# Kernel tuning notes

Hardware: AMD Instinct MI355X
Metric: run time of the kernel (lower is better)

Reference implementation:

```python
import jax, jax.numpy as jnp
import numpy as np

DIM = 2048
HEADS = 16
HD = DIM // HEADS  # 128
EPS = 1e-5


def layernorm(t, w, b):
    # FloatLayerNorm: LayerNorm computed in float32 over last dim
    t32 = t.astype(jnp.float32)
    mu = jnp.mean(t32, axis=-1, keepdims=True)
    var = jnp.mean(jnp.square(t32 - mu), axis=-1, keepdims=True)
    y = (t32 - mu) * jax.lax.rsqrt(var + EPS)
    return (y * w + b).astype(t.dtype)


def rope(t, f_real, f_imag):
    # t: [b, s, h, hd]; frequencies in cis form, sliced to seq length
    b, s, h, hd = t.shape
    tr = t.astype(jnp.float32).reshape(b, s, h, hd // 2, 2)
    xr, xi = tr[..., 0], tr[..., 1]
    fr = f_real[:s][None, :, None, :]  # [1, s, 1, hd/2]
    fi = f_imag[:s][None, :, None, :]
    o_r = xr * fr - xi * fi
    o_i = xr * fi + xi * fr
    return jnp.stack([o_r, o_i], axis=-1).reshape(b, s, h, hd).astype(t.dtype)


def proj_norm_rope(t, Wq, Wk, Wv, qn_w, qn_b, kn_w, kn_b, f_real, f_imag):
    b, s, _ = t.shape
    q = layernorm(t @ Wq, qn_w, qn_b).reshape(b, s, HEADS, HD)
    k = layernorm(t @ Wk, kn_w, kn_b).reshape(b, s, HEADS, HD)
    v = (t @ Wv).reshape(b, s, HEADS, HD)
    q = rope(q, f_real, f_imag)
    k = rope(k, f_real, f_imag)
    return q, k, v


def sdpa(q, k, v, scale):
    # q,k,v: [b, s, h, hd] -> out [b, s, h, hd]
    scores = jnp.einsum('bqhd,bkhd->bhqk', q, k) * scale
    probs = jax.nn.softmax(scores, axis=-1)
    return jnp.einsum('bhqk,bkhd->bqhd', probs, v)


def setup_inputs() -> dict:
    key = jax.random.key(0)
    ks = jax.random.split(key, 14)
    d = {
        'c': jax.random.normal(ks[0], (2, 256, DIM), jnp.float32),
        'x': jax.random.normal(ks[1], (2, 1792, DIM), jnp.float32),
        'f_real': jax.random.normal(ks[2], (2048, HD // 2), jnp.float32),
        'f_imag': jax.random.normal(ks[3], (2048, HD // 2), jnp.float32),
    }
    sc = 1.0 / np.sqrt(DIM)
    for i, name in enumerate(['Wq', 'Wk', 'Wv', 'Wo', 'W2q', 'W2k', 'W2v', 'W2o']):
        d[name] = jax.random.normal(ks[4 + i], (DIM, DIM), jnp.float32) * sc
    for name in ['qn_w', 'kn_w', 'q2n_w', 'k2n_w']:
        d[name] = jnp.ones((DIM,), jnp.float32)
    for name in ['qn_b', 'kn_b', 'q2n_b', 'k2n_b']:
        d[name] = jnp.zeros((DIM,), jnp.float32)
    return d


def reference(c, x, f_real, f_imag, Wq, Wk, Wv, Wo, W2q, W2k, W2v, W2o,
              qn_w, qn_b, kn_w, kn_b, q2n_w, q2n_b, k2n_w, k2n_b):
    s1 = c.shape[1]
    c_q, c_k, c_v = proj_norm_rope(c, Wq, Wk, Wv, qn_w, qn_b, kn_w, kn_b, f_real, f_imag)
    x_q, x_k, x_v = proj_norm_rope(x, W2q, W2k, W2v, q2n_w, q2n_b, k2n_w, k2n_b, f_real, f_imag)
    q = jnp.concatenate([c_q, x_q], axis=1)
    k = jnp.concatenate([c_k, x_k], axis=1)
    v = jnp.concatenate([c_v, x_v], axis=1)
    out = sdpa(q, k, v, scale=1.0 / np.sqrt(HD))  # scale_by_num_heads=True
    b, s, _, _ = out.shape
    out = out.reshape(b, s, DIM)
    c_out = out[:, :s1] @ Wo
    x_out = out[:, s1:] @ W2o
    return c_out, x_out
```

## Files before the change

### kernel.cpp

```cpp
#include <hip/hip_runtime.h>

typedef __attribute__((ext_vector_type(8))) short short8;
typedef __attribute__((ext_vector_type(4))) float f32x4;
typedef __attribute__((ext_vector_type(16))) float f32x16;

#define DEV __device__ __forceinline__

DEV unsigned short f2bf(float f) {
  unsigned int u; __builtin_memcpy(&u, &f, 4);
  u = (u + 0x7FFFu + ((u >> 16) & 1u)) >> 16;
  return (unsigned short)u;
}
DEV float bf2f(unsigned short h) {
  unsigned int u = ((unsigned int)h) << 16;
  float f; __builtin_memcpy(&f, &u, 4);
  return f;
}
DEV unsigned int cvtpk(float lo, float hi_) {
  unsigned int r;
  asm("v_cvt_pk_bf16_f32 %0, %1, %2" : "=v"(r) : "v"(lo), "v"(hi_));
  return r;
}

DEV void gload_lds16(const void* g, void* l) {
  __builtin_amdgcn_global_load_lds(
      (const __attribute__((address_space(1))) void*)g,
      (__attribute__((address_space(3))) void*)l, 16, 0, 0);
}

DEV f32x16 mfma32(short8 a, short8 b, f32x16 c) {
  return __builtin_amdgcn_mfma_f32_32x32x16_bf16(a, b, c, 0, 0, 0);
}
DEV f32x4 mfma16(short8 a, short8 b, f32x4 c) {
  return __builtin_amdgcn_mfma_f32_16x16x32_bf16(a, b, c, 0, 0, 0);
}

__global__ __launch_bounds__(256) void conv_tb(const float* __restrict__ c,
                                               const float* __restrict__ x,
                                               unsigned short* __restrict__ tb) {
  int row = blockIdx.x;
  int b = row >> 11, s = row & 2047;
  const float* src = (s < 256) ? (c + (size_t)(b * 256 + s) * 2048)
                               : (x + (size_t)(b * 1792 + (s - 256)) * 2048);
  int t = threadIdx.x;
  float4 v0 = *(const float4*)&src[t * 8];
  float4 v1 = *(const float4*)&src[t * 8 + 4];
  union { unsigned short us[8]; uint4 u; } pk;
  pk.us[0] = f2bf(v0.x); pk.us[1] = f2bf(v0.y); pk.us[2] = f2bf(v0.z); pk.us[3] = f2bf(v0.w);
  pk.us[4] = f2bf(v1.x); pk.us[5] = f2bf(v1.y); pk.us[6] = f2bf(v1.z); pk.us[7] = f2bf(v1.w);
  *(uint4*)&tb[(size_t)row * 2048 + t * 8] = pk.u;
}

__global__ __launch_bounds__(256) void trans_w(
    const float* __restrict__ w0, const float* __restrict__ w1,
    const float* __restrict__ w2, const float* __restrict__ w3,
    const float* __restrict__ w4, const float* __restrict__ w5,
    const float* __restrict__ w6, const float* __restrict__ w7,
    unsigned short* __restrict__ dstbase) {
  const float* W;
  switch (blockIdx.z) {
    case 0: W = w0; break; case 1: W = w1; break; case 2: W = w2; break; case 3: W = w3; break;
    case 4: W = w4; break; case 5: W = w5; break; case 6: W = w6; break; default: W = w7; break;
  }
  unsigned short* Wt = dstbase + (size_t)blockIdx.z * 2048 * 2048;
  __shared__ float tile[64][65];
  int n0 = blockIdx.x * 64, k0 = blockIdx.y * 64;
  int j = threadIdx.x & 63, i0 = threadIdx.x >> 6;
#pragma unroll
  for (int p = 0; p < 16; ++p) {
    int i = i0 + p * 4;
    tile[i][j] = W[(size_t)(k0 + i) * 2048 + n0 + j];
  }
  __syncthreads();
#pragma unroll
  for (int p = 0; p < 16; ++p) {
    int i = i0 + p * 4;
    Wt[(size_t)(n0 + i) * 2048 + k0 + j] = f2bf(tile[j][i]);
  }
}

DEV void stage_A8(char* ldsAbase, const unsigned short* gtile, int mh, int wid, int lane) {
#pragma unroll
  for (int p = 0; p < 2; ++p) {
    int row0 = mh * 64 + p * 128 + wid * 8;
    int row = row0 + (lane >> 3);
    int u = (lane & 7) ^ (row & 7);
    gload_lds16(gtile + (size_t)row * 2048 + u * 8, ldsAbase + row0 * 128);
  }
}
DEV void stage_B8(char* ldsBbase, const unsigned short* gtile, int nh, int wid, int lane) {
#pragma unroll
  for (int p = 0; p < 2; ++p) {
    int idx = p * 8 + wid;
    int row0 = (idx >> 2) * 64 + nh * 32 + (idx & 3) * 8;
    int row = row0 + (lane >> 3);
    int u = (lane & 7) ^ (row & 7);
    gload_lds16(gtile + (size_t)row * 2048 + u * 8, ldsBbase + row0 * 128);
  }
}

__global__ __launch_bounds__(512, 2) void gemm_qkv3_8ph(
    const unsigned short* __restrict__ A,
    const unsigned short* __restrict__ Wt,
    unsigned short* __restrict__ out) {
  extern __shared__ __align__(16) char ldsc[];
  const size_t M2 = 2048ull * 2048ull;
  int bid = blockIdx.x;
  int sw = (bid & 7) * 48 + (bid >> 3);
  const int which = sw >> 7;
  const int rem = sw & 127;
  const int m0 = (rem >> 3) * 256, n0 = (rem & 7) * 256;
  const unsigned short* Bt = Wt + (size_t)(((m0 & 2047) < 256) ? which : which + 4) * M2;
  unsigned short* C = out + (size_t)which * (4096ull * 2048ull);
  const int tid = threadIdx.x, wid = tid >> 6, lane = tid & 63;
  const int l31 = lane & 31, hi = lane >> 5;
  const int wm = wid >> 2, wn = wid & 3;
  const unsigned short* gA = A + (size_t)m0 * 2048;
  const unsigned short* gB = Bt + (size_t)n0 * 2048;

  f32x16 acc[4][2] = {};
  short8 af[2][4], bf0[4], bf1[4];

#define READ_AF(Abase, mh)                                                           \
  _Pragma("unroll") for (int mt = 0; mt < 2; ++mt)                                   \
  _Pragma("unroll") for (int s = 0; s < 4; ++s) {                                    \
    int row = wm * 128 + (mh) * 64 + mt * 32 + l31;                                  \
    af[mt][s] = *(const short8*)((Abase) + row * 128 + (((s * 2 + hi) ^ (row & 7)) << 4)); \
  }
#define READ_BF(Bbase, nh, dst)                                                      \
  _Pragma("unroll") for (int s = 0; s < 4; ++s) {                                    \
    int row = wn * 64 + (nh) * 32 + l31;                                             \
    dst[s] = *(const short8*)((Bbase) + row * 128 + (((s * 2 + hi) ^ (row & 7)) << 4)); \
  }
#define MFMA_Q(mhb, BF, nh)                                                          \
  _Pragma("unroll") for (int mt = 0; mt < 2; ++mt)                                   \
  _Pragma("unroll") for (int s = 0; s < 4; ++s)                                      \
    acc[(mhb) * 2 + mt][nh] = mfma32(af[mt][s], BF[s], acc[(mhb) * 2 + mt][nh]);

  stage_A8(ldsc, gA, 0, wid, lane);
  stage_A8(ldsc, gA, 1, wid, lane);
  stage_B8(ldsc + 32768, gB, 0, wid, lane);
  stage_B8(ldsc + 32768, gB, 1, wid, lane);
  stage_A8(ldsc + 65536, gA + 64, 0, wid, lane);
  stage_B8(ldsc + 98304, gB + 64, 0, wid, lane);
  asm volatile("s_waitcnt vmcnt(4)" ::: "memory");
  __builtin_amdgcn_s_barrier();

  const int NT = 32;
#pragma unroll 1
  for (int t = 0; t < NT; ++t) {
    const int bufOff = (t & 1) << 16;
    char* Ab = ldsc + bufOff;
    char* Bb = ldsc + 32768 + bufOff;
    char* An = ldsc + (bufOff ^ 65536);
    char* Bn = ldsc + 32768 + (bufOff ^ 65536);

    READ_AF(Ab, 0)
    READ_BF(Bb, 0, bf0)
    if (t + 1 < NT) stage_B8(Bn, gB + (t + 1) * 64, 1, wid, lane);
    __builtin_amdgcn_s_barrier();
    asm volatile("s_waitcnt lgkmcnt(0)" ::: "memory");
    __builtin_amdgcn_sched_barrier(0);
    __builtin_amdgcn_s_setprio(1);
    MFMA_Q(0, bf0, 0)
    __builtin_amdgcn_s_setprio(0);
    __builtin_amdgcn_s_barrier();

    READ_BF(Bb, 1, bf1)
    if (t + 1 < NT) stage_A8(An, gA + (t + 1) * 64, 1, wid, lane);
    __builtin_amdgcn_s_barrier();
    asm volatile("s_waitcnt lgkmcnt(0)" ::: "memory");
    __builtin_amdgcn_sched_barrier(0);
    __builtin_amdgcn_s_setprio(1);
    MFMA_Q(0, bf1, 1)
    __builtin_amdgcn_s_setprio(0);
    __builtin_amdgcn_s_barrier();

    READ_AF(Ab, 1)
    if (t + 2 < NT) stage_A8(Ab, gA + (t + 2) * 64, 0, wid, lane);
    __builtin_amdgcn_s_barrier();
    asm volatile("s_waitcnt lgkmcnt(0)" ::: "memory");
    __builtin_amdgcn_sched_barrier(0);
    __builtin_amdgcn_s_setprio(1);
    MFMA_Q(1, bf0, 0)
    __builtin_amdgcn_s_setprio(0);
    __builtin_amdgcn_s_barrier();

    if (t + 2 < NT) stage_B8(Bb, gB + (t + 2) * 64, 0, wid, lane);
    __builtin_amdgcn_s_barrier();
    __builtin_amdgcn_s_setprio(1);
    MFMA_Q(1, bf1, 1)
    __builtin_amdgcn_s_setprio(0);
    if (t + 2 < NT) {
      asm volatile("s_waitcnt vmcnt(4)" ::: "memory");
    } else if (t + 1 < NT) {
      asm volatile("s_waitcnt vmcnt(0)" ::: "memory");
    }
    __builtin_amdgcn_s_barrier();
  }

#pragma unroll
  for (int q = 0; q < 4; ++q) {
    int base_row = m0 + wm * 128 + (q >> 1) * 64 + (q & 1) * 32;
#pragma unroll
    for (int nh = 0; nh < 2; ++nh) {
      int col = n0 + wn * 64 + nh * 32 + l31;
#pragma unroll
      for (int reg = 0; reg < 16; ++reg) {
        int row = base_row + (reg & 3) + 8 * (reg >> 2) + 4 * hi;
        C[(size_t)row * 2048 + col] = f2bf(acc[q][nh][reg]);
      }
    }
  }
#undef READ_AF
#undef READ_BF
#undef MFMA_Q
}

__global__ __launch_bounds__(256) void gemm_out(
    const unsigned short* __restrict__ A,
    const unsigned short* __restrict__ B1t,
    const unsigned short* __restrict__ B2t,
    float* __restrict__ Co) {
  __shared__ __align__(16) unsigned short As[128 * 32];
  __shared__ __align__(16) unsigned short Bs[128 * 32];
  const int m0 = blockIdx.y * 128, n0 = blockIdx.x * 128;
  const unsigned short* Bt = ((m0 & 2047) < 256) ? B1t : B2t;
  const int tid = threadIdx.x, wid = tid >> 6, lane = tid & 63;
  const int g = lane >> 4, l15 = lane & 15;
  const int wm = wid >> 1, wn = wid & 1;
  const int srow = lane >> 2, skk = (lane & 3) * 8;
  f32x4 acc[4][4] = {};
  for (int k0 = 0; k0 < 2048; k0 += 32) {
#pragma unroll
    for (int rep = 0; rep < 2; ++rep) {
      int ia = wid * 2 + rep;
      gload_lds16(&A[(size_t)(m0 + ia * 16 + srow) * 2048 + k0 + skk], (char*)As + ia * 1024);
      gload_lds16(&Bt[(size_t)(n0 + ia * 16 + srow) * 2048 + k0 + skk], (char*)Bs + ia * 1024);
    }
    __syncthreads();
    short8 a[4], bb[4];
#pragma unroll
    for (int mf = 0; mf < 4; ++mf) a[mf] = *(const short8*)&As[(wm * 64 + mf * 16 + l15) * 32 + g * 8];
#pragma unroll
    for (int nf = 0; nf < 4; ++nf) bb[nf] = *(const short8*)&Bs[(wn * 64 + nf * 16 + l15) * 32 + g * 8];
#pragma unroll
    for (int mf = 0; mf < 4; ++mf)
#pragma unroll
      for (int nf = 0; nf < 4; ++nf)
        acc[mf][nf] = mfma16(a[mf], bb[nf], acc[mf][nf]);
    __syncthreads();
  }
#pragma unroll
  for (int mf = 0; mf < 4; ++mf)
#pragma unroll
    for (int r = 0; r < 4; ++r) {
      int row = m0 + wm * 64 + mf * 16 + 4 * g + r;
      int b = row >> 11, s = row & 2047;
      size_t dst = (s < 256) ? ((size_t)b * 256 + s) * 2048
                             : 1048576ull + ((size_t)b * 1792 + (s - 256)) * 2048;
#pragma unroll
      for (int nf = 0; nf < 4; ++nf)
        Co[dst + n0 + wn * 64 + nf * 16 + l15] = acc[mf][nf][r];
    }
}

__global__ __launch_bounds__(256) void ln_rope(
    const unsigned short* __restrict__ P,
    const float* __restrict__ w1, const float* __restrict__ b1,
    const float* __restrict__ w2, const float* __restrict__ b2,
    const float* __restrict__ fre, const float* __restrict__ fim,
    unsigned short* __restrict__ Oa, float oscale) {
  int row = blockIdx.x;
  int b = row >> 11, s = row & 2047;
  int pos = (s < 256) ? s : s - 256;
  const float* w = (s < 256) ? w1 : w2;
  const float* bb = (s < 256) ? b1 : b2;
  int t = threadIdx.x, lane = t & 63, wid = t >> 6;
  int col = t * 8;
  uint4 raw = *(const uint4*)&P[(size_t)row * 2048 + col];
  const unsigned short* rp = (const unsigned short*)&raw;
  float xv[8];
#pragma unroll
  for (int j = 0; j < 8; ++j) xv[j] = bf2f(rp[j]);
  float s1 = 0.f, s2 = 0.f;
#pragma unroll
  for (int j = 0; j < 8; ++j) { s1 += xv[j]; s2 += xv[j] * xv[j]; }
#pragma unroll
  for (int off = 32; off; off >>= 1) { s1 += __shfl_xor(s1, off); s2 += __shfl_xor(s2, off); }
  __shared__ float red1[4], red2[4];
  if (lane == 0) { red1[wid] = s1; red2[wid] = s2; }
  __syncthreads();
  s1 = red1[0] + red1[1] + red1[2] + red1[3];
  s2 = red2[0] + red2[1] + red2[2] + red2[3];
  float mean = s1 * (1.f / 2048.f);
  float var = s2 * (1.f / 2048.f) - mean * mean;
  float rs = rsqrtf(var + 1e-5f);
  float4 wv0 = *(const float4*)&w[col], wv1 = *(const float4*)&w[col + 4];
  float4 bv0 = *(const float4*)&bb[col], bv1 = *(const float4*)&bb[col + 4];
  float y[8];
  y[0] = (xv[0] - mean) * rs * wv0.x + bv0.x; y[1] = (xv[1] - mean) * rs * wv0.y + bv0.y;
  y[2] = (xv[2] - mean) * rs * wv0.z + bv0.z; y[3] = (xv[3] - mean) * rs * wv0.w + bv0.w;
  y[4] = (xv[4] - mean) * rs * wv1.x + bv1.x; y[5] = (xv[5] - mean) * rs * wv1.y + bv1.y;
  y[6] = (xv[6] - mean) * rs * wv1.z + bv1.z; y[7] = (xv[7] - mean) * rs * wv1.w + bv1.w;
#pragma unroll
  for (int j = 0; j < 8; ++j) y[j] *= oscale;
  int hd0 = col & 127;
  int i0 = hd0 >> 1;
  float4 fr = *(const float4*)&fre[(size_t)pos * 64 + i0];
  float4 fi = *(const float4*)&fim[(size_t)pos * 64 + i0];
  union { unsigned short us[8]; uint4 u; } pk;
  pk.us[0] = f2bf(y[0] * fr.x - y[1] * fi.x); pk.us[1] = f2bf(y[0] * fi.x + y[1] * fr.x);
  pk.us[2] = f2bf(y[2] * fr.y - y[3] * fi.y); pk.us[3] = f2bf(y[2] * fi.y + y[3] * fr.y);
  pk.us[4] = f2bf(y[4] * fr.z - y[5] * fi.z); pk.us[5] = f2bf(y[4] * fi.z + y[5] * fr.z);
  pk.us[6] = f2bf(y[6] * fr.w - y[7] * fi.w); pk.us[7] = f2bf(y[6] * fi.w + y[7] * fr.w);
  int h = col >> 7;
  *(uint4*)&Oa[((size_t)(b * 16 + h) * 2048 + s) * 128 + hd0] = pk.u;
}

__global__ __launch_bounds__(256) void v_trans(const unsigned short* __restrict__ vp,
                                               unsigned short* __restrict__ va) {
  int bh = blockIdx.y;
  int b = bh >> 4, h = bh & 15;
  int s0 = blockIdx.x * 64;
  __shared__ unsigned short tile[64][128];
  int tid = threadIdx.x;
#pragma unroll
  for (int p = 0; p < 4; ++p) {
    int s = p * 16 + (tid >> 4);
    int d0 = (tid & 15) * 8;
    *(uint4*)&tile[s][d0] = *(const uint4*)&vp[((size_t)b * 2048 + s0 + s) * 2048 + h * 128 + d0];
  }
  __syncthreads();
#pragma unroll
  for (int p = 0; p < 4; ++p) {
    int d = p * 32 + (tid >> 3);
    int soff = (tid & 7) * 8;
    union { unsigned short us[8]; uint4 u; } pk;
#pragma unroll
    for (int u = 0; u < 8; ++u) pk.us[u] = tile[soff + u][d];
    *(uint4*)&va[((size_t)(b * 16 + h) * 128 + d) * 2048 + s0 + soff] = pk.u;
  }
}

#define THR_LOG2 11.5f

__global__ __launch_bounds__(512) void attn_kernel(
    const unsigned short* __restrict__ Q,
    const unsigned short* __restrict__ Kb,
    const unsigned short* __restrict__ Vt,
    unsigned short* __restrict__ O) {
  __shared__ __align__(16) unsigned short smem[32768];
  const int q0 = blockIdx.x * 256;
  const int h = blockIdx.y, b = blockIdx.z;
  const int tid = threadIdx.x, wid = tid >> 6, lane = tid & 63;
  const int l31 = lane & 31, hi = lane >> 5;
  const size_t base = (size_t)(b * 16 + h) * 2048 * 128;
  const unsigned short* kbase = Kb + base;
  const unsigned short* vbase = Vt + base;

  const int qrow = q0 + wid * 32 + l31;
  short8 qf[8];
#pragma unroll
  for (int ks = 0; ks < 8; ++ks)
    qf[ks] = *(const short8*)&Q[base + (size_t)qrow * 128 + ks * 16 + hi * 8];

  f32x16 o_acc[4] = {};
  float m_run = -1e30f, l_run = 0.f;

#define STAGE(cur, kv0)                                                              \
  {                                                                                  \
_Pragma("unroll")                                                                    \
    for (int p = 0; p < 2; ++p) {                                                    \
      int slot = p * 512 + wid * 64 + lane;                                          \
      int row = slot >> 4;                                                           \
      int u = (slot & 15) ^ (row & 7);                                               \
      gload_lds16(&kbase[(size_t)((kv0) + row) * 128 + u * 8],                       \
                  (char*)(smem + (cur) * 16384) + (p * 512 + wid * 64) * 16);        \
    }                                                                                \
_Pragma("unroll")                                                                    \
    for (int p = 0; p < 2; ++p) {                                                    \
      int slot = p * 512 + wid * 64 + lane;                                          \
      int d = slot >> 3;                                                             \
      int u = (slot & 7) ^ (d & 7);                                                  \
      gload_lds16(&vbase[(size_t)d * 2048 + (kv0) + u * 8],                          \
                  (char*)(smem + (cur) * 16384 + 8192) + (p * 512 + wid * 64) * 16); \
    }                                                                                \
  }

  STAGE(0, 0)

#pragma unroll 1
  for (int t = 0; t < 32; ++t) {
    const int cur = t & 1;
    if (t < 31) {
      STAGE(cur ^ 1, (t + 1) * 64)
      asm volatile("s_waitcnt vmcnt(4)" ::: "memory");
    } else {
      asm volatile("s_waitcnt vmcnt(0)" ::: "memory");
    }
    __builtin_amdgcn_s_barrier();

    const char* Ksb = (const char*)(smem + cur * 16384);
    const char* Vsb = (const char*)(smem + cur * 16384 + 8192);

    f32x16 sT0 = {}, sT1 = {};
    __builtin_amdgcn_s_setprio(1);
#pragma unroll
    for (int ks = 0; ks < 8; ++ks) {
      int unit = ks * 2 + hi;
      int r0 = l31;
      short8 kf0 = *(const short8*)(Ksb + ((r0 * 16 + (unit ^ (r0 & 7))) << 4));
      sT0 = mfma32(kf0, qf[ks], sT0);
      int r1 = 32 + l31;
      short8 kf1 = *(const short8*)(Ksb + ((r1 * 16 + (unit ^ (r1 & 7))) << 4));
      sT1 = mfma32(kf1, qf[ks], sT1);
    }
    __builtin_amdgcn_s_setprio(0);

    float mx = sT0[0];
#pragma unroll
    for (int r = 1; r < 16; ++r) mx = fmaxf(mx, sT0[r]);
#pragma unroll
    for (int r = 0; r < 16; ++r) mx = fmaxf(mx, sT1[r]);
    mx = fmaxf(mx, __shfl_xor(mx, 32));
    if (!__all(mx <= m_run + THR_LOG2)) {
      float mn = fmaxf(m_run, mx);
      float corr = __builtin_exp2f(m_run - mn);
      m_run = mn;
      l_run *= corr;
#pragma unroll
      for (int di = 0; di < 4; ++di)
#pragma unroll
        for (int r = 0; r < 16; ++r) o_acc[di][r] *= corr;
    }
    float ts = 0.f;
#pragma unroll
    for (int r = 0; r < 16; ++r) { sT0[r] = __builtin_exp2f(sT0[r] - m_run); ts += sT0[r]; }
#pragma unroll
    for (int r = 0; r < 16; ++r) { sT1[r] = __builtin_exp2f(sT1[r] - m_run); ts += sT1[r]; }
    ts += __shfl_xor(ts, 32);
    l_run += ts;

    unsigned int w0[8], w1[8];
#pragma unroll
    for (int j = 0; j < 8; ++j) {
      w0[j] = cvtpk(sT0[2 * j], sT0[2 * j + 1]);
      w1[j] = cvtpk(sT1[2 * j], sT1[2 * j + 1]);
    }
    unsigned int y0[4], y1[4];
    y0[0] = __shfl_xor((int)(hi ? w0[0] : w0[2]), 32);
    y0[1] = __shfl_xor((int)(hi ? w0[1] : w0[3]), 32);
    y0[2] = __shfl_xor((int)(hi ? w0[4] : w0[6]), 32);
    y0[3] = __shfl_xor((int)(hi ? w0[5] : w0[7]), 32);
    y1[0] = __shfl_xor((int)(hi ? w1[0] : w1[2]), 32);
    y1[1] = __shfl_xor((int)(hi ? w1[1] : w1[3]), 32);
    y1[2] = __shfl_xor((int)(hi ? w1[4] : w1[6]), 32);
    y1[3] = __shfl_xor((int)(hi ? w1[5] : w1[7]), 32);
    union { unsigned int u[4]; short8 s8; } pf[2][2];
    pf[0][0].u[0] = hi ? y0[0] : w0[0]; pf[0][0].u[1] = hi ? y0[1] : w0[1];
    pf[0][0].u[2] = hi ? w0[2] : y0[0]; pf[0][0].u[3] = hi ? w0[3] : y0[1];
    pf[0][1].u[0] = hi ? y0[2] : w0[4]; pf[0][1].u[1] = hi ? y0[3] : w0[5];
    pf[0][1].u[2] = hi ? w0[6] : y0[2]; pf[0][1].u[3] = hi ? w0[7] : y0[3];
    pf[1][0].u[0] = hi ? y1[0] : w1[0]; pf[1][0].u[1] = hi ? y1[1] : w1[1];
    pf[1][0].u[2] = hi ? w1[2] : y1[0]; pf[1][0].u[3] = hi ? w1[3] : y1[1];
    pf[1][1].u[0] = hi ? y1[2] : w1[4]; pf[1][1].u[1] = hi ? y1[3] : w1[5];
    pf[1][1].u[2] = hi ? w1[6] : y1[2]; pf[1][1].u[3] = hi ? w1[7] : y1[3];

    __builtin_amdgcn_s_setprio(1);
#pragma unroll
    for (int di = 0; di < 4; ++di) {
      int row = di * 32 + l31;
      int sw = row & 7;
#pragma unroll
      for (int kb = 0; kb < 2; ++kb)
#pragma unroll
        for (int ks2 = 0; ks2 < 2; ++ks2) {
          int unit = kb * 4 + ks2 * 2 + hi;
          short8 vf = *(const short8*)(Vsb + ((row * 8 + (unit ^ sw)) << 4));
          o_acc[di] = mfma32(vf, pf[kb][ks2].s8, o_acc[di]);
        }
    }
    __builtin_amdgcn_s_setprio(0);
    __builtin_amdgcn_s_barrier();
  }

  float inv = 1.0f / l_run;
  char* ow = (char*)smem + wid * 8192;
#pragma unroll
  for (int di = 0; di < 4; ++di)
#pragma unroll
    for (int rg = 0; rg < 4; ++rg) {
      unsigned int lo = cvtpk(o_acc[di][rg * 4 + 0] * inv, o_acc[di][rg * 4 + 1] * inv);
      unsigned int hi_w = cvtpk(o_acc[di][rg * 4 + 2] * inv, o_acc[di][rg * 4 + 3] * inv);
      int byte = (l31 * 256 + di * 64 + rg * 16 + hi * 8) ^ ((l31 & 7) << 4);
      *(unsigned long long*)(ow + byte) =
          ((unsigned long long)hi_w << 32) | (unsigned long long)lo;
    }
  size_t obase = ((size_t)b * 2048 + q0 + wid * 32) * 2048 + (size_t)h * 128;
#pragma unroll
  for (int it = 0; it < 8; ++it) {
    int q = it * 4 + (lane >> 4);
    int d0 = (lane & 15) * 8;
    int byte = (q * 256 + d0 * 2) ^ ((q & 7) << 4);
    uint4 val = *(const uint4*)(ow + byte);
    *(uint4*)&O[obase + (size_t)q * 2048 + d0] = val;
  }
}

extern "C" void kernel_launch(void* const* d_in, const int* in_sizes, int n_in,
                              void* d_out, int out_size, void* d_ws, size_t ws_size,
                              hipStream_t stream) {
  (void)in_sizes; (void)n_in; (void)out_size; (void)ws_size;
  const float* c = (const float*)d_in[0];
  const float* x = (const float*)d_in[1];
  const float* fre = (const float*)d_in[2];
  const float* fim = (const float*)d_in[3];

  char* ws = (char*)d_ws;
  const size_t M2 = 2048ull * 2048ull;
  unsigned short* tb = (unsigned short*)ws;
  unsigned short* Wt = (unsigned short*)(ws + 16777216ull);
  unsigned short* qkv = (unsigned short*)(ws + 83886080ull);
  unsigned short* qp = qkv;
  unsigned short* kp = (unsigned short*)(ws + 100663296ull);
  unsigned short* vp = (unsigned short*)(ws + 117440512ull);
  unsigned short* qa = (unsigned short*)(ws + 134217728ull);
  unsigned short* ka = (unsigned short*)(ws + 150994944ull);
  unsigned short* va = (unsigned short*)(ws + 167772160ull);
  unsigned short* attn_out = qp;

  (void)hipFuncSetAttribute((const void*)gemm_qkv3_8ph,
                            hipFuncAttributeMaxDynamicSharedMemorySize, 131072);

  conv_tb<<<4096, 256, 0, stream>>>(c, x, tb);
  trans_w<<<dim3(32, 32, 8), 256, 0, stream>>>(
      (const float*)d_in[4], (const float*)d_in[5], (const float*)d_in[6], (const float*)d_in[7],
      (const float*)d_in[8], (const float*)d_in[9], (const float*)d_in[10], (const float*)d_in[11],
      Wt);
  gemm_qkv3_8ph<<<384, 512, 131072, stream>>>(tb, Wt, qkv);
  ln_rope<<<4096, 256, 0, stream>>>(qp, (const float*)d_in[12], (const float*)d_in[16],
                                    (const float*)d_in[14], (const float*)d_in[18], fre, fim, qa,
                                    0.08838834764831845f * 1.4426950408889634f);
  ln_rope<<<4096, 256, 0, stream>>>(kp, (const float*)d_in[13], (const float*)d_in[17],
                                    (const float*)d_in[15], (const float*)d_in[19], fre, fim, ka,
                                    1.0f);
  v_trans<<<dim3(32, 32), 256, 0, stream>>>(vp, va);
  attn_kernel<<<dim3(8, 16, 2), 512, 0, stream>>>(qa, ka, va, attn_out);
  gemm_out<<<dim3(16, 32), 256, 0, stream>>>(attn_out, Wt + 3 * M2, Wt + 7 * M2, (float*)d_out);
}
```

Baseline: 352.8 us.

## Deepen attention KV prefetch, merge q/k ln_rope launches, refine GEMM LDS swizzle

The attention kernel moves from a two-buffer to a four-buffer dynamic-LDS ring with two tiles in flight. This lets it drop the trailing barrier per iteration and hide more load latency. The Q and K layernorm+rope launches are merged into one 8192-block kernel to save a launch and the tail between them. The QKV GEMM LDS swizzle gains an extra XOR bit from row bit 3 to cut bank conflicts. The risks are lower attention occupancy from 128KB of LDS per block, and a possible race from removing the barrier, since buffer reuse now relies on the ring being three tiles deep.

```diff
diff --git a/kernel.cpp b/kernel.cpp
--- a/kernel.cpp
+++ b/kernel.cpp
@@ -34,6 +34,8 @@
 DEV f32x4 mfma16(short8 a, short8 b, f32x4 c) {
   return __builtin_amdgcn_mfma_f32_16x16x32_bf16(a, b, c, 0, 0, 0);
 }
+
+DEV int USW(int u, int row) { return u ^ (row & 7) ^ (((row >> 3) & 1) << 1); }
 
 __global__ __launch_bounds__(256) void conv_tb(const float* __restrict__ c,
                                                const float* __restrict__ x,
@@ -84,7 +86,7 @@
   for (int p = 0; p < 2; ++p) {
     int row0 = mh * 64 + p * 128 + wid * 8;
     int row = row0 + (lane >> 3);
-    int u = (lane & 7) ^ (row & 7);
+    int u = USW(lane & 7, row);
     gload_lds16(gtile + (size_t)row * 2048 + u * 8, ldsAbase + row0 * 128);
   }
 }
@@ -94,7 +96,7 @@
     int idx = p * 8 + wid;
     int row0 = (idx >> 2) * 64 + nh * 32 + (idx & 3) * 8;
     int row = row0 + (lane >> 3);
-    int u = (lane & 7) ^ (row & 7);
+    int u = USW(lane & 7, row);
     gload_lds16(gtile + (size_t)row * 2048 + u * 8, ldsBbase + row0 * 128);
   }
 }
@@ -125,12 +127,12 @@
   _Pragma("unroll") for (int mt = 0; mt < 2; ++mt)                                   \
   _Pragma("unroll") for (int s = 0; s < 4; ++s) {                                    \
     int row = wm * 128 + (mh) * 64 + mt * 32 + l31;                                  \
-    af[mt][s] = *(const short8*)((Abase) + row * 128 + (((s * 2 + hi) ^ (row & 7)) << 4)); \
+    af[mt][s] = *(const short8*)((Abase) + row * 128 + (USW(s * 2 + hi, row) << 4)); \
   }
 #define READ_BF(Bbase, nh, dst)                                                      \
   _Pragma("unroll") for (int s = 0; s < 4; ++s) {                                    \
     int row = wn * 64 + (nh) * 32 + l31;                                             \
-    dst[s] = *(const short8*)((Bbase) + row * 128 + (((s * 2 + hi) ^ (row & 7)) << 4)); \
+    dst[s] = *(const short8*)((Bbase) + row * 128 + (USW(s * 2 + hi, row) << 4));    \
   }
 #define MFMA_Q(mhb, BF, nh)                                                          \
   _Pragma("unroll") for (int mt = 0; mt < 2; ++mt)                                   \
@@ -265,17 +267,24 @@
     }
 }
 
-__global__ __launch_bounds__(256) void ln_rope(
+__global__ __launch_bounds__(256) void ln_rope2(
     const unsigned short* __restrict__ P,
-    const float* __restrict__ w1, const float* __restrict__ b1,
-    const float* __restrict__ w2, const float* __restrict__ b2,
+    const float* __restrict__ qw1, const float* __restrict__ qb1,
+    const float* __restrict__ qw2, const float* __restrict__ qb2,
+    const float* __restrict__ kw1, const float* __restrict__ kb1,
+    const float* __restrict__ kw2, const float* __restrict__ kb2,
     const float* __restrict__ fre, const float* __restrict__ fim,
-    unsigned short* __restrict__ Oa, float oscale) {
-  int row = blockIdx.x;
+    unsigned short* __restrict__ Oa, float qscale) {
+  int gid = blockIdx.x;
+  int mat = gid >> 12;
+  int row = gid & 4095;
+  P += (size_t)mat * 8388608ull;
+  Oa += (size_t)mat * 8388608ull;
+  float oscale = mat ? 1.0f : qscale;
   int b = row >> 11, s = row & 2047;
   int pos = (s < 256) ? s : s - 256;
-  const float* w = (s < 256) ? w1 : w2;
-  const float* bb = (s < 256) ? b1 : b2;
+  const float* w = (s < 256) ? (mat ? kw1 : qw1) : (mat ? kw2 : qw2);
+  const float* bb = (s < 256) ? (mat ? kb1 : qb1) : (mat ? kb2 : qb2);
   int t = threadIdx.x, lane = t & 63, wid = t >> 6;
   int col = t * 8;
   uint4 raw = *(const uint4*)&P[(size_t)row * 2048 + col];
@@ -350,7 +359,7 @@
     const unsigned short* __restrict__ Kb,
     const unsigned short* __restrict__ Vt,
     unsigned short* __restrict__ O) {
-  __shared__ __align__(16) unsigned short smem[32768];
+  extern __shared__ __align__(16) char asmem[];
   const int q0 = blockIdx.x * 256;
   const int h = blockIdx.y, b = blockIdx.z;
   const int tid = threadIdx.x, wid = tid >> 6, lane = tid & 63;
@@ -368,7 +377,7 @@
   f32x16 o_acc[4] = {};
   float m_run = -1e30f, l_run = 0.f;
 
-#define STAGE(cur, kv0)                                                              \
+#define STAGE(bufi, kv0)                                                             \
   {                                                                                  \
 _Pragma("unroll")                                                                    \
     for (int p = 0; p < 2; ++p) {                                                    \
@@ -376,7 +385,7 @@
       int row = slot >> 4;                                                           \
       int u = (slot & 15) ^ (row & 7);                                               \
       gload_lds16(&kbase[(size_t)((kv0) + row) * 128 + u * 8],                       \
-                  (char*)(smem + (cur) * 16384) + (p * 512 + wid * 64) * 16);        \
+                  asmem + (bufi) * 32768 + (p * 512 + wid * 64) * 16);               \
     }                                                                                \
 _Pragma("unroll")                                                                    \
     for (int p = 0; p < 2; ++p) {                                                    \
@@ -384,25 +393,27 @@
       int d = slot >> 3;                                                             \
       int u = (slot & 7) ^ (d & 7);                                                  \
       gload_lds16(&vbase[(size_t)d * 2048 + (kv0) + u * 8],                          \
-                  (char*)(smem + (cur) * 16384 + 8192) + (p * 512 + wid * 64) * 16); \
+                  asmem + (bufi) * 32768 + 16384 + (p * 512 + wid * 64) * 16);       \
     }                                                                                \
   }
 
   STAGE(0, 0)
+  STAGE(1, 64)
 
 #pragma unroll 1
   for (int t = 0; t < 32; ++t) {
-    const int cur = t & 1;
-    if (t < 31) {
-      STAGE(cur ^ 1, (t + 1) * 64)
+    if (t + 2 < 32) {
+      STAGE((t + 2) & 3, (t + 2) * 64)
+      asm volatile("s_waitcnt vmcnt(8)" ::: "memory");
+    } else if (t + 1 < 32) {
       asm volatile("s_waitcnt vmcnt(4)" ::: "memory");
     } else {
       asm volatile("s_waitcnt vmcnt(0)" ::: "memory");
     }
     __builtin_amdgcn_s_barrier();
 
-    const char* Ksb = (const char*)(smem + cur * 16384);
-    const char* Vsb = (const char*)(smem + cur * 16384 + 8192);
+    const char* Ksb = asmem + (t & 3) * 32768;
+    const char* Vsb = Ksb + 16384;
 
     f32x16 sT0 = {}, sT1 = {};
     __builtin_amdgcn_s_setprio(1);
@@ -482,11 +493,10 @@
         }
     }
     __builtin_amdgcn_s_setprio(0);
-    __builtin_amdgcn_s_barrier();
   }
 
   float inv = 1.0f / l_run;
-  char* ow = (char*)smem + wid * 8192;
+  char* ow = asmem + wid * 8192;
 #pragma unroll
   for (int di = 0; di < 4; ++di)
 #pragma unroll
@@ -497,6 +507,7 @@
       *(unsigned long long*)(ow + byte) =
           ((unsigned long long)hi_w << 32) | (unsigned long long)lo;
     }
+  asm volatile("s_waitcnt lgkmcnt(0)" ::: "memory");
   size_t obase = ((size_t)b * 2048 + q0 + wid * 32) * 2048 + (size_t)h * 128;
 #pragma unroll
   for (int it = 0; it < 8; ++it) {
@@ -523,7 +534,6 @@
   unsigned short* Wt = (unsigned short*)(ws + 16777216ull);
   unsigned short* qkv = (unsigned short*)(ws + 83886080ull);
   unsigned short* qp = qkv;
-  unsigned short* kp = (unsigned short*)(ws + 100663296ull);
   unsigned short* vp = (unsigned short*)(ws + 117440512ull);
   unsigned short* qa = (unsigned short*)(ws + 134217728ull);
   unsigned short* ka = (unsigned short*)(ws + 150994944ull);
@@ -531,6 +541,8 @@
   unsigned short* attn_out = qp;
 
   (void)hipFuncSetAttribute((const void*)gemm_qkv3_8ph,
+                            hipFuncAttributeMaxDynamicSharedMemorySize, 131072);
+  (void)hipFuncSetAttribute((const void*)attn_kernel,
                             hipFuncAttributeMaxDynamicSharedMemorySize, 131072);
 
   conv_tb<<<4096, 256, 0, stream>>>(c, x, tb);
@@ -539,13 +551,14 @@
       (const float*)d_in[8], (const float*)d_in[9], (const float*)d_in[10], (const float*)d_in[11],
       Wt);
   gemm_qkv3_8ph<<<384, 512, 131072, stream>>>(tb, Wt, qkv);
-  ln_rope<<<4096, 256, 0, stream>>>(qp, (const float*)d_in[12], (const float*)d_in[16],
-                                    (const float*)d_in[14], (const float*)d_in[18], fre, fim, qa,
-                                    0.08838834764831845f * 1.4426950408889634f);
-  ln_rope<<<4096, 256, 0, stream>>>(kp, (const float*)d_in[13], (const float*)d_in[17],
-                                    (const float*)d_in[15], (const float*)d_in[19], fre, fim, ka,
-                                    1.0f);
+  ln_rope2<<<8192, 256, 0, stream>>>(qp,
+                                     (const float*)d_in[12], (const float*)d_in[16],
+                                     (const float*)d_in[14], (const float*)d_in[18],
+                                     (const float*)d_in[13], (const float*)d_in[17],
+                                     (const float*)d_in[15], (const float*)d_in[19],
+                                     fre, fim, qa,
+                                     0.08838834764831845f * 1.4426950408889634f);
   v_trans<<<dim3(32, 32), 256, 0, stream>>>(vp, va);
-  attn_kernel<<<dim3(8, 16, 2), 512, 0, stream>>>(qa, ka, va, attn_out);
+  attn_kernel<<<dim3(8, 16, 2), 512, 131072, stream>>>(qa, ka, va, attn_out);
   gemm_out<<<dim3(16, 32), 256, 0, stream>>>(attn_out, Wt + 3 * M2, Wt + 7 * M2, (float*)d_out);
 }
```

New measurement: 363.5 us. +3.0%, slower.
